# Optimization experiments

Measured on AMD Instinct MI355X. Metric: run time of the kernel, lower is better.

## Reference

```python
import jax, jax.numpy as jnp
import numpy as np

B = 4096
N = 256  # num_input_feat


def setup_inputs() -> dict:
    key = jax.random.key(0)
    k1, k2, k3 = jax.random.split(key, 3)
    x = jax.random.normal(k1, (B, N), dtype=jnp.float32)
    weight_w = jax.random.normal(k2, (N,), dtype=jnp.float32)
    weight_b = jax.random.normal(k3, (N,), dtype=jnp.float32)
    return {"x": x, "weight_w": weight_w, "weight_b": weight_b}


def reference(x, weight_w, weight_b):
    # elementwise affine on features: feat = x * w + b  -> (B, N)
    feat = x * weight_w + weight_b
    # batched outer product: (B,N,1) @ (B,1,N) -> (B,N,N)
    Z = jnp.einsum('bi,bj->bij', feat, feat)
    b, n = x.shape
    num_ints = n * (n + 1) // 2
    # faithful to original: take the FIRST n(n+1)/2 entries of row-major flatten
    return Z.reshape(b, n * n)[:, :num_ints]
```

## Files before the change

kernel.cpp:

```cpp
#include <hip/hip_runtime.h>


#define NFEAT 256
#define NOUT  32896

typedef float f32x4 __attribute__((ext_vector_type(4)));

__global__ __launch_bounds__(256) void dot_outer_kernel(
    const float* __restrict__ x,
    const float* __restrict__ w,
    const float* __restrict__ bias,
    float* __restrict__ out)
{
    __shared__ float feat[NFEAT];
    const int b = blockIdx.x;
    const int t = threadIdx.x;

    feat[t] = x[(size_t)b * NFEAT + t] * w[t] + bias[t];
    __syncthreads();

    const f32x4* feat4 = (const f32x4*)feat;
    f32x4* out4 = (f32x4*)(out + (size_t)b * NOUT);

    const f32x4 fj = feat4[t & 63];

    #pragma unroll
    for (int iter = 0; iter < 32; ++iter) {
        const int idx = iter * 256 + t;
        const float fi = feat[idx >> 6];
        f32x4 v;
        v.x = fi * fj.x;
        v.y = fi * fj.y;
        v.z = fi * fj.z;
        v.w = fi * fj.w;
        __builtin_nontemporal_store(v, &out4[idx]);
    }

    if (t < 32) {
        const float fi = feat[128];
        const f32x4 fjt = feat4[t];
        f32x4 v;
        v.x = fi * fjt.x;
        v.y = fi * fjt.y;
        v.z = fi * fjt.z;
        v.w = fi * fjt.w;
        __builtin_nontemporal_store(v, &out4[8192 + t]);
    }
}

extern "C" void kernel_launch(void* const* d_in, const int* in_sizes, int n_in,
                              void* d_out, int out_size, void* d_ws, size_t ws_size,
                              hipStream_t stream) {
    const float* x    = (const float*)d_in[0];
    const float* w    = (const float*)d_in[1];
    const float* bias = (const float*)d_in[2];
    float* out = (float*)d_out;

    const int B = in_sizes[0] / NFEAT;
    dot_outer_kernel<<<B, 256, 0, stream>>>(x, w, bias, out);
}
```

Before: 528.4 us.

## Map one wavefront per batch row and broadcast features via readlane

```diff
diff --git a/kernel.cpp b/kernel.cpp
--- a/kernel.cpp
+++ b/kernel.cpp
@@ -6,45 +6,60 @@
 
 typedef float f32x4 __attribute__((ext_vector_type(4)));
 
+__device__ __forceinline__ float readlane_f(float v, int lane) {
+    return __builtin_bit_cast(float,
+        __builtin_amdgcn_readlane(__builtin_bit_cast(int, v), lane));
+}
+
 __global__ __launch_bounds__(256) void dot_outer_kernel(
     const float* __restrict__ x,
     const float* __restrict__ w,
     const float* __restrict__ bias,
     float* __restrict__ out)
 {
-    __shared__ float feat[NFEAT];
-    const int b = blockIdx.x;
-    const int t = threadIdx.x;
+    const int t    = threadIdx.x;
+    const int lane = t & 63;
+    const int wid  = t >> 6;
+    const int b    = (blockIdx.x << 2) + wid;
 
-    feat[t] = x[(size_t)b * NFEAT + t] * w[t] + bias[t];
-    __syncthreads();
+    const f32x4 xv = *(const f32x4*)(x    + (size_t)b * NFEAT + 4 * lane);
+    const f32x4 wv = *(const f32x4*)(w    + 4 * lane);
+    const f32x4 bv = *(const f32x4*)(bias + 4 * lane);
 
-    const f32x4* feat4 = (const f32x4*)feat;
-    f32x4* out4 = (f32x4*)(out + (size_t)b * NOUT);
+    f32x4 f;
+    f.x = xv.x * wv.x + bv.x;
+    f.y = xv.y * wv.y + bv.y;
+    f.z = xv.z * wv.z + bv.z;
+    f.w = xv.w * wv.w + bv.w;
 
-    const f32x4 fj = feat4[t & 63];
+    f32x4* outw = (f32x4*)(out + (size_t)b * NOUT) + lane;
 
     #pragma unroll
-    for (int iter = 0; iter < 32; ++iter) {
-        const int idx = iter * 256 + t;
-        const float fi = feat[idx >> 6];
+    for (int i = 0; i < 128; ++i) {
+        float comp;
+        switch (i & 3) {
+            case 0:  comp = f.x; break;
+            case 1:  comp = f.y; break;
+            case 2:  comp = f.z; break;
+            default: comp = f.w; break;
+        }
+        const float fi = readlane_f(comp, i >> 2);
         f32x4 v;
-        v.x = fi * fj.x;
-        v.y = fi * fj.y;
-        v.z = fi * fj.z;
-        v.w = fi * fj.w;
-        __builtin_nontemporal_store(v, &out4[idx]);
+        v.x = fi * f.x;
+        v.y = fi * f.y;
+        v.z = fi * f.z;
+        v.w = fi * f.w;
+        __builtin_nontemporal_store(v, outw + (size_t)i * 64);
     }
 
-    if (t < 32) {
-        const float fi = feat[128];
-        const f32x4 fjt = feat4[t];
+    const float fi = readlane_f(f.x, 32);
+    if (lane < 32) {
         f32x4 v;
-        v.x = fi * fjt.x;
-        v.y = fi * fjt.y;
-        v.z = fi * fjt.z;
-        v.w = fi * fjt.w;
-        __builtin_nontemporal_store(v, &out4[8192 + t]);
+        v.x = fi * f.x;
+        v.y = fi * f.y;
+        v.z = fi * f.z;
+        v.w = fi * f.w;
+        __builtin_nontemporal_store(v, outw + 128 * 64);
     }
 }
 
@@ -57,5 +72,5 @@
     float* out = (float*)d_out;
 
     const int B = in_sizes[0] / NFEAT;
-    dot_outer_kernel<<<B, 256, 0, stream>>>(x, w, bias, out);
+    dot_outer_kernel<<<B / 4, 256, 0, stream>>>(x, w, bias, out);
 }
```

New measurement: 529.4 us. No clear change (+0.2%).
